# Performance work log

Hardware: AMD Instinct MI355X
Metric: run time of the kernel (lower is better)

The kernel has to match this reference:

```python
import jax, jax.numpy as jnp
import numpy as np

BLOCK_SIZE = 32
# NVFP4 decode table: index bit3 = sign, bits0-2 = magnitude code
DECODE = jnp.array([0.0, 0.5, 1.0, 1.5, 2.0, 3.0, 4.0, 6.0,
                    -0.0, -0.5, -1.0, -1.5, -2.0, -3.0, -4.0, -6.0], dtype=jnp.float32)

N_OUT, K_IN = 16384, 4096


def setup_inputs() -> dict:
    key = jax.random.key(0)
    k1, k2, k3, k4 = jax.random.split(key, 4)
    x = jax.random.normal(k1, (4, 512, K_IN), dtype=jnp.float32)
    # packed uint8 stored as int32 in [0, 256)
    weight_packed = jax.random.randint(k2, (N_OUT, K_IN // 2), 0, 256, dtype=jnp.int32)
    # per-block positive scales (block_max / 6.0 in the original)
    weight_scales = jax.random.uniform(k3, (N_OUT, K_IN // BLOCK_SIZE), dtype=jnp.float32,
                                       minval=1e-3, maxval=5e-2)
    bias = jax.random.normal(k4, (N_OUT,), dtype=jnp.float32) * 0.02
    return {"x": x, "weight_packed": weight_packed, "weight_scales": weight_scales, "bias": bias}


def _dequant(weight_packed, weight_scales):
    # unpack: low nibble -> even K index, high nibble -> odd K index
    low = DECODE[weight_packed & 15]           # [N, K//2]
    high = DECODE[(weight_packed >> 4) & 15]   # [N, K//2]
    n = weight_packed.shape[0]
    w = jnp.stack([low, high], axis=-1).reshape(n, -1)  # [N, K], interleaved
    # expand per-block scales along K
    scales = jnp.repeat(weight_scales, BLOCK_SIZE, axis=1)  # [N, K]
    return w * scales


def reference(x, weight_packed, weight_scales, bias):
    w = _dequant(weight_packed, weight_scales)            # [N, K]
    out = jnp.einsum('bsk,nk->bsn', x, w) + bias          # [B, S, N]
    # activation='gelu' -> F.gelu(approximate='tanh')
    return jax.nn.gelu(out, approximate=True)
```

## Files before the change

kernel.cpp:

```cpp
#include <hip/hip_runtime.h>
#include <hip/hip_bf16.h>

typedef short bf16x8 __attribute__((ext_vector_type(8)));
typedef float f32x4 __attribute__((ext_vector_type(4)));

#define K_DIM 4096
#define N_DIM 16384
#define M_DIM 2048
#define STRIPE 16384
#define TSTRIDE (64 * STRIPE)
#define WSB_BYTES ((size_t)N_DIM * K_DIM * 2)
#define WSA_BYTES ((size_t)M_DIM * K_DIM * 2)

__device__ __forceinline__ unsigned f2bf(float f) {
    unsigned u = __builtin_bit_cast(unsigned, f);
    u += 0x7FFFu + ((u >> 16) & 1u);
    return u >> 16;
}

__device__ __forceinline__ float dec4(unsigned c, float s) {
    unsigned mag = c & 7u;
    unsigned u = (mag >= 2u) ? ((((mag >> 1) + 126u) << 23) | ((mag & 1u) << 22))
                             : (mag == 1u ? 0x3F000000u : 0u);
    u |= (c & 8u) << 28;
    return __builtin_bit_cast(float, u) * s;
}

__device__ __forceinline__ float gelu_tanh(float v) {
    float c = v + 0.044715f * v * v * v;
    float t = tanhf(0.7978845608028654f * c);
    return 0.5f * v * (1.0f + t);
}

__global__ __launch_bounds__(256) void dequant_w(const int* __restrict__ wp,
                                                 const float* __restrict__ wsc,
                                                 unsigned char* __restrict__ dst) {
    int t = blockIdx.x * 256 + threadIdx.x;
    int n = t >> 9;
    int ck = t & 511;
    int kstep = ck >> 3, s = ck & 7;
    int nt = n >> 7, r = n & 127;

    const int4 p4 = *reinterpret_cast<const int4*>(wp + (size_t)n * (K_DIM / 2) + kstep * 32 + s * 4);
    float scale = wsc[(size_t)n * (K_DIM / 32) + kstep * 2 + (s >> 2)];

    const int pv[4] = {p4.x, p4.y, p4.z, p4.w};
    unsigned o[8];
    #pragma unroll
    for (int j = 0; j < 4; ++j) {
        unsigned b = (unsigned)pv[j] & 255u;
        o[2 * j]     = f2bf(dec4(b & 15u, scale));
        o[2 * j + 1] = f2bf(dec4((b >> 4) & 15u, scale));
    }
    uint4 v;
    v.x = o[0] | (o[1] << 16);
    v.y = o[2] | (o[3] << 16);
    v.z = o[4] | (o[5] << 16);
    v.w = o[6] | (o[7] << 16);

    size_t off = (size_t)(nt * 64 + kstep) * STRIPE
               + (size_t)r * 128 + (size_t)((s ^ (r & 7)) << 4);
    *reinterpret_cast<uint4*>(dst + off) = v;
}

__global__ __launch_bounds__(256) void conv_x(const float* __restrict__ x,
                                              unsigned char* __restrict__ dst) {
    int t = blockIdx.x * 256 + threadIdx.x;
    int m = t >> 9;
    int ck = t & 511;
    int kstep = ck >> 3, s = ck & 7;
    int mt = m >> 7, r = m & 127;

    const float4* xp = reinterpret_cast<const float4*>(x + (size_t)m * K_DIM + kstep * 64 + s * 8);
    float4 a = xp[0], b = xp[1];
    uint4 v;
    v.x = f2bf(a.x) | (f2bf(a.y) << 16);
    v.y = f2bf(a.z) | (f2bf(a.w) << 16);
    v.z = f2bf(b.x) | (f2bf(b.y) << 16);
    v.w = f2bf(b.z) | (f2bf(b.w) << 16);

    size_t off = (size_t)(mt * 64 + kstep) * STRIPE
               + (size_t)r * 128 + (size_t)((s ^ (r & 7)) << 4);
    *reinterpret_cast<uint4*>(dst + off) = v;
}


__global__ __launch_bounds__(512, 2) void gemm_bf16_256(
    const unsigned char* __restrict__ wsA,
    const unsigned char* __restrict__ wsB,
    const float* __restrict__ bias,
    float* __restrict__ out)
{
    __shared__ unsigned char lds[131072];

    int id = blockIdx.x;
    int wg = (id & 7) * 64 + (id >> 3);
    int MT = wg & 7;
    int NT = wg >> 3;

    const int tid  = threadIdx.x;
    const int lane = tid & 63;
    const int w    = tid >> 6;
    const int wm   = w >> 2;
    const int wn   = w & 3;
    const int fr   = lane & 15;
    const int fg   = lane >> 4;

    const unsigned char* gA = wsA + (size_t)(2 * MT) * TSTRIDE;
    const unsigned char* gB = wsB + (size_t)(2 * NT) * TSTRIDE;

    int addrA[8];
    #pragma unroll
    for (int mi = 0; mi < 8; ++mi) {
        int row = wm * 128 + mi * 16 + fr;
        int L = row >> 1;
        addrA[mi] = L * 128 + (((((row & 1) << 2) | fg) ^ (L & 7)) << 4);
    }
    int addrB[4];
    #pragma unroll
    for (int ni = 0; ni < 4; ++ni) {
        int row = wn * 64 + ni * 16 + fr;
        int L = row >> 1;
        addrB[ni] = L * 128 + (((((row & 1) << 2) | fg) ^ (L & 7)) << 4);
    }

    int offST[2][2];
    #pragma unroll
    for (int j = 0; j < 2; ++j) {
        int c = w * 2 + j;
        int L = c * 8 + (lane >> 3);
        int p = lane & 7;
        int sl = p ^ (L & 7);
        int h = sl >> 2, fgs = sl & 3;
        int row = 2 * L + h;
        #pragma unroll
        for (int kb = 0; kb < 2; ++kb)
            offST[j][kb] = (row >> 7) * TSTRIDE + (row & 127) * 128
                         + ((((kb << 2) | fgs) ^ (row & 7)) << 4);
    }

#define GLDS(SRC, DOFF) __builtin_amdgcn_global_load_lds(                          \
        (const __attribute__((address_space(1))) unsigned int*)(SRC),              \
        (__attribute__((address_space(3))) unsigned int*)(&lds[DOFF]), 16, 0, 0)

#define STAGE_A(KSOFF, KB, SLOT) do {                                              \
        GLDS(gA + (KSOFF) + offST[0][KB], ((SLOT) << 14) + (w * 2 + 0) * 1024);    \
        GLDS(gA + (KSOFF) + offST[1][KB], ((SLOT) << 14) + (w * 2 + 1) * 1024);    \
    } while (0)
#define STAGE_B(KSOFF, KB, SLOT) do {                                              \
        GLDS(gB + (KSOFF) + offST[0][KB], 65536 + ((SLOT) << 14) + (w * 2 + 0) * 1024); \
        GLDS(gB + (KSOFF) + offST[1][KB], 65536 + ((SLOT) << 14) + (w * 2 + 1) * 1024); \
    } while (0)

    f32x4 acc[8][4];
    #pragma unroll
    for (int mi = 0; mi < 8; ++mi)
        #pragma unroll
        for (int ni = 0; ni < 4; ++ni)
            acc[mi][ni] = (f32x4){0.f, 0.f, 0.f, 0.f};

    STAGE_A(0, 0, 0);        STAGE_B(0, 0, 0);
    STAGE_A(0, 1, 1);        STAGE_B(0, 1, 1);
    STAGE_A(STRIPE, 0, 2);   STAGE_B(STRIPE, 0, 2);
    asm volatile("s_waitcnt vmcnt(8)" ::: "memory");
    __builtin_amdgcn_sched_barrier(0);
    __builtin_amdgcn_s_barrier();
    __builtin_amdgcn_sched_barrier(0);

#define TILE_BODY(RSLOT, DO_STG, STKS, STKB, SSLOT, VMN) do {                      \
        const unsigned char* la = lds + ((RSLOT) << 14);                           \
        const unsigned char* lb = lds + 65536 + ((RSLOT) << 14);                   \
        bf16x8 bfr[4], af[4];                                                      \
        if (DO_STG) STAGE_A(STKS, STKB, SSLOT);                                    \
        _Pragma("unroll") for (int ni = 0; ni < 4; ++ni)                           \
            bfr[ni] = *reinterpret_cast<const bf16x8*>(lb + addrB[ni]);            \
        _Pragma("unroll") for (int mi = 0; mi < 4; ++mi)                           \
            af[mi] = *reinterpret_cast<const bf16x8*>(la + addrA[mi]);             \
        __builtin_amdgcn_s_setprio(1);                                             \
        _Pragma("unroll") for (int mi = 0; mi < 4; ++mi)                           \
            _Pragma("unroll") for (int ni = 0; ni < 4; ++ni)                       \
                acc[mi][ni] = __builtin_amdgcn_mfma_f32_16x16x32_bf16(             \
                    af[mi], bfr[ni], acc[mi][ni], 0, 0, 0);                        \
        __builtin_amdgcn_s_setprio(0);                                             \
        if (DO_STG) STAGE_B(STKS, STKB, SSLOT);                                    \
        _Pragma("unroll") for (int mi = 0; mi < 4; ++mi)                           \
            af[mi] = *reinterpret_cast<const bf16x8*>(la + addrA[4 + mi]);         \
        __builtin_amdgcn_s_setprio(1);                                             \
        _Pragma("unroll") for (int mi = 0; mi < 4; ++mi)                           \
            _Pragma("unroll") for (int ni = 0; ni < 4; ++ni)                       \
                acc[4 + mi][ni] = __builtin_amdgcn_mfma_f32_16x16x32_bf16(         \
                    af[mi], bfr[ni], acc[4 + mi][ni], 0, 0, 0);                    \
        __builtin_amdgcn_s_setprio(0);                                             \
        if ((VMN) >= 0) {                                                          \
            if ((VMN) == 8)      asm volatile("s_waitcnt vmcnt(8)" ::: "memory");  \
            else if ((VMN) == 4) asm volatile("s_waitcnt vmcnt(4)" ::: "memory");  \
            else                 asm volatile("s_waitcnt vmcnt(0)" ::: "memory");  \
            __builtin_amdgcn_sched_barrier(0);                                     \
            __builtin_amdgcn_s_barrier();                                          \
            __builtin_amdgcn_sched_barrier(0);                                     \
        }                                                                          \
    } while (0)

    for (int tp = 0; tp < 62; ++tp) {
        const int scur = (tp & 1) << 1;
        const int ks1 = (tp + 1) * STRIPE;
        const int ks2 = (tp + 2) * STRIPE;
        TILE_BODY(scur,     1, ks1, 1, scur ^ 3, 8);
        TILE_BODY(scur ^ 1, 1, ks2, 0, scur,     8);
    }
    TILE_BODY(0, 1, 63 * STRIPE, 1, 3, 8);
    TILE_BODY(1, 0, 0, 0, 0, 4);
    TILE_BODY(2, 0, 0, 0, 0, 0);
    TILE_BODY(3, 0, 0, 0, 0, -1);

    const int bm0 = MT * 256, bn0 = NT * 256;
    #pragma unroll
    for (int mi = 0; mi < 8; ++mi) {
        int row = bm0 + wm * 128 + mi * 16 + fg * 4;
        #pragma unroll
        for (int ni = 0; ni < 4; ++ni) {
            int col = bn0 + wn * 64 + ni * 16 + fr;
            float bv = bias[col];
            float* op = out + (size_t)row * N_DIM + col;
            #pragma unroll
            for (int q = 0; q < 4; ++q) {
                float v = acc[mi][ni][q] + bv;
                op[(size_t)q * N_DIM] = gelu_tanh(v);
            }
        }
    }
#undef TILE_BODY
#undef STAGE_A
#undef STAGE_B
#undef GLDS
}

__global__ __launch_bounds__(256, 2) void nvfp4_gemm(
    const float* __restrict__ x,
    const int*   __restrict__ wp,
    const float* __restrict__ wscale,
    const float* __restrict__ bias,
    float* __restrict__ out)
{
    __shared__ uint4  lsA[128 * 8];
    __shared__ uint4  lsB[128 * 8];
    __shared__ float2 lut[256];

    const int tid = threadIdx.x;
    {
        static const float dectab[16] = {0.f, 0.5f, 1.f, 1.5f, 2.f, 3.f, 4.f, 6.f,
                                         -0.f,-0.5f,-1.f,-1.5f,-2.f,-3.f,-4.f,-6.f};
        lut[tid] = make_float2(dectab[tid & 15], dectab[(tid >> 4) & 15]);
    }

    const int bn0 = blockIdx.x * 128;
    const int bm0 = blockIdx.y * 128;
    const int r = tid >> 1;
    const int h = tid & 1;

    const float4* xp = reinterpret_cast<const float4*>(x + (size_t)(bm0 + r) * K_DIM) + h * 8;
    const uint4*  bp = reinterpret_cast<const uint4*>(wp + (size_t)(bn0 + r) * (K_DIM / 2)) + h * 4;
    const float*  sp = wscale + (size_t)(bn0 + r) * (K_DIM / 32) + h;

    float4 ax[8];
    uint4  bx[4];
    float  scale;
    #pragma unroll
    for (int j = 0; j < 8; ++j) ax[j] = xp[j];
    #pragma unroll
    for (int q = 0; q < 4; ++q) bx[q] = bp[q];
    scale = sp[0];

    f32x4 acc[4][4];
    #pragma unroll
    for (int mi = 0; mi < 4; ++mi)
        #pragma unroll
        for (int ni = 0; ni < 4; ++ni)
            acc[mi][ni] = (f32x4){0.f, 0.f, 0.f, 0.f};

    const int lane = tid & 63;
    const int wid  = tid >> 6;
    const int wm0  = (wid >> 1) * 64;
    const int wn0  = (wid & 1) * 64;
    const int fr   = lane & 15;
    const int fg   = lane >> 4;

    __syncthreads();

    for (int kt = 0; kt < 64; ++kt) {
        #pragma unroll
        for (int j = 0; j < 4; ++j) {
            float4 f0 = ax[2 * j], f1 = ax[2 * j + 1];
            uint4 v;
            v.x = f2bf(f0.x) | (f2bf(f0.y) << 16);
            v.y = f2bf(f0.z) | (f2bf(f0.w) << 16);
            v.z = f2bf(f1.x) | (f2bf(f1.y) << 16);
            v.w = f2bf(f1.z) | (f2bf(f1.w) << 16);
            lsA[(r * 8 + h * 4 + j) ^ (r & 7)] = v;
        }
        #pragma unroll
        for (int q = 0; q < 4; ++q) {
            uint4 p = bx[q];
            float2 d0 = lut[p.x & 255];
            float2 d1 = lut[p.y & 255];
            float2 d2 = lut[p.z & 255];
            float2 d3 = lut[p.w & 255];
            uint4 v;
            v.x = f2bf(d0.x * scale) | (f2bf(d0.y * scale) << 16);
            v.y = f2bf(d1.x * scale) | (f2bf(d1.y * scale) << 16);
            v.z = f2bf(d2.x * scale) | (f2bf(d2.y * scale) << 16);
            v.w = f2bf(d3.x * scale) | (f2bf(d3.y * scale) << 16);
            lsB[(r * 8 + h * 4 + q) ^ (r & 7)] = v;
        }
        __syncthreads();

        if (kt + 1 < 64) {
            #pragma unroll
            for (int j = 0; j < 8; ++j) ax[j] = xp[(kt + 1) * 16 + j];
            #pragma unroll
            for (int q = 0; q < 4; ++q) bx[q] = bp[(kt + 1) * 8 + q];
            scale = sp[(kt + 1) * 2];
        }

        #pragma unroll
        for (int kk = 0; kk < 2; ++kk) {
            bf16x8 af[4], bfr[4];
            #pragma unroll
            for (int mi = 0; mi < 4; ++mi) {
                int row = wm0 + mi * 16 + fr;
                af[mi] = __builtin_bit_cast(bf16x8, lsA[(row * 8 + kk * 4 + fg) ^ (row & 7)]);
            }
            #pragma unroll
            for (int ni = 0; ni < 4; ++ni) {
                int row = wn0 + ni * 16 + fr;
                bfr[ni] = __builtin_bit_cast(bf16x8, lsB[(row * 8 + kk * 4 + fg) ^ (row & 7)]);
            }
            #pragma unroll
            for (int mi = 0; mi < 4; ++mi)
                #pragma unroll
                for (int ni = 0; ni < 4; ++ni)
                    acc[mi][ni] = __builtin_amdgcn_mfma_f32_16x16x32_bf16(
                        af[mi], bfr[ni], acc[mi][ni], 0, 0, 0);
        }
        __syncthreads();
    }

    #pragma unroll
    for (int mi = 0; mi < 4; ++mi) {
        int row = bm0 + wm0 + mi * 16 + fg * 4;
        #pragma unroll
        for (int ni = 0; ni < 4; ++ni) {
            int col = bn0 + wn0 + ni * 16 + fr;
            float bv = bias[col];
            float* op = out + (size_t)row * N_DIM + col;
            #pragma unroll
            for (int q = 0; q < 4; ++q) {
                float v = acc[mi][ni][q] + bv;
                op[(size_t)q * N_DIM] = gelu_tanh(v);
            }
        }
    }
}

extern "C" void kernel_launch(void* const* d_in, const int* in_sizes, int n_in,
                              void* d_out, int out_size, void* d_ws, size_t ws_size,
                              hipStream_t stream) {
    const float* x    = (const float*)d_in[0];
    const int*   wp   = (const int*)d_in[1];
    const float* wsc  = (const float*)d_in[2];
    const float* bias = (const float*)d_in[3];
    float*       out  = (float*)d_out;
    (void)in_sizes; (void)n_in; (void)out_size;

    if (ws_size >= WSB_BYTES + WSA_BYTES) {
        unsigned char* wsB = (unsigned char*)d_ws;
        unsigned char* wsA = wsB + WSB_BYTES;
        dequant_w<<<(N_DIM * (K_DIM / 8)) / 256, 256, 0, stream>>>(wp, wsc, wsB);
        conv_x<<<(M_DIM * (K_DIM / 8)) / 256, 256, 0, stream>>>(x, wsA);
        gemm_bf16_256<<<(M_DIM / 256) * (N_DIM / 256), 512, 0, stream>>>(wsA, wsB, bias, out);
    } else {
        dim3 grid(N_DIM / 128, M_DIM / 128);
        nvfp4_gemm<<<grid, 256, 0, stream>>>(x, wp, wsc, bias, out);
    }
}
```

Before: 322.3 us.

## Prefetch next tile's LDS fragments into registers during current tile's MFMAs

Software-pipelines the LDS-to-register reads in the bf16 GEMM main loop. The B fragments and the first half of the A fragments for the next k-slot are read into a second register set while the current slot's second MFMA batch runs. This hides LDS read latency behind matrix instructions. It tightens the global-load waits (vmcnt 8 to 4) so the next slot is resident one tile earlier, which may expose more global-load latency. It also raises VGPR pressure under the 2-wave occupancy bound.

```diff
diff --git a/kernel.cpp b/kernel.cpp
--- a/kernel.cpp
+++ b/kernel.cpp
@@ -152,48 +152,55 @@
         GLDS(gB + (KSOFF) + offST[1][KB], 65536 + ((SLOT) << 14) + (w * 2 + 1) * 1024); \
     } while (0)
 
+#define READ_PF(PA, PB, SLOT) do {                                                 \
+        const unsigned char* La_ = lds + ((SLOT) << 14);                           \
+        const unsigned char* Lb_ = lds + 65536 + ((SLOT) << 14);                   \
+        _Pragma("unroll") for (int ni = 0; ni < 4; ++ni)                           \
+            PB[ni] = *reinterpret_cast<const bf16x8*>(Lb_ + addrB[ni]);            \
+        _Pragma("unroll") for (int mi = 0; mi < 4; ++mi)                           \
+            PA[mi] = *reinterpret_cast<const bf16x8*>(La_ + addrA[mi]);            \
+    } while (0)
+
     f32x4 acc[8][4];
     #pragma unroll
     for (int mi = 0; mi < 8; ++mi)
         #pragma unroll
         for (int ni = 0; ni < 4; ++ni)
             acc[mi][ni] = (f32x4){0.f, 0.f, 0.f, 0.f};
+
+    bf16x8 pa0[4], pb0[4], pa1[4], pb1[4];
 
     STAGE_A(0, 0, 0);        STAGE_B(0, 0, 0);
     STAGE_A(0, 1, 1);        STAGE_B(0, 1, 1);
     STAGE_A(STRIPE, 0, 2);   STAGE_B(STRIPE, 0, 2);
-    asm volatile("s_waitcnt vmcnt(8)" ::: "memory");
+    asm volatile("s_waitcnt vmcnt(4)" ::: "memory");
     __builtin_amdgcn_sched_barrier(0);
     __builtin_amdgcn_s_barrier();
     __builtin_amdgcn_sched_barrier(0);
-
-#define TILE_BODY(RSLOT, DO_STG, STKS, STKB, SSLOT, VMN) do {                      \
+    READ_PF(pa0, pb0, 0);
+
+#define TILE_BODY(RSLOT, NSLOT, PA, PB, NPA, NPB, DO_STG, STKS, STKB, SSLOT, DO_PF, VMN) do { \
         const unsigned char* la = lds + ((RSLOT) << 14);                           \
-        const unsigned char* lb = lds + 65536 + ((RSLOT) << 14);                   \
-        bf16x8 bfr[4], af[4];                                                      \
+        bf16x8 ka[4];                                                              \
         if (DO_STG) STAGE_A(STKS, STKB, SSLOT);                                    \
-        _Pragma("unroll") for (int ni = 0; ni < 4; ++ni)                           \
-            bfr[ni] = *reinterpret_cast<const bf16x8*>(lb + addrB[ni]);            \
         _Pragma("unroll") for (int mi = 0; mi < 4; ++mi)                           \
-            af[mi] = *reinterpret_cast<const bf16x8*>(la + addrA[mi]);             \
+            ka[mi] = *reinterpret_cast<const bf16x8*>(la + addrA[4 + mi]);         \
         __builtin_amdgcn_s_setprio(1);                                             \
         _Pragma("unroll") for (int mi = 0; mi < 4; ++mi)                           \
             _Pragma("unroll") for (int ni = 0; ni < 4; ++ni)                       \
                 acc[mi][ni] = __builtin_amdgcn_mfma_f32_16x16x32_bf16(             \
-                    af[mi], bfr[ni], acc[mi][ni], 0, 0, 0);                        \
+                    PA[mi], PB[ni], acc[mi][ni], 0, 0, 0);                         \
         __builtin_amdgcn_s_setprio(0);                                             \
         if (DO_STG) STAGE_B(STKS, STKB, SSLOT);                                    \
-        _Pragma("unroll") for (int mi = 0; mi < 4; ++mi)                           \
-            af[mi] = *reinterpret_cast<const bf16x8*>(la + addrA[4 + mi]);         \
+        if (DO_PF) READ_PF(NPA, NPB, NSLOT);                                       \
         __builtin_amdgcn_s_setprio(1);                                             \
         _Pragma("unroll") for (int mi = 0; mi < 4; ++mi)                           \
             _Pragma("unroll") for (int ni = 0; ni < 4; ++ni)                       \
                 acc[4 + mi][ni] = __builtin_amdgcn_mfma_f32_16x16x32_bf16(         \
-                    af[mi], bfr[ni], acc[4 + mi][ni], 0, 0, 0);                    \
+                    ka[mi], PB[ni], acc[4 + mi][ni], 0, 0, 0);                     \
         __builtin_amdgcn_s_setprio(0);                                             \
         if ((VMN) >= 0) {                                                          \
-            if ((VMN) == 8)      asm volatile("s_waitcnt vmcnt(8)" ::: "memory");  \
-            else if ((VMN) == 4) asm volatile("s_waitcnt vmcnt(4)" ::: "memory");  \
+            if ((VMN) == 4)      asm volatile("s_waitcnt vmcnt(4)" ::: "memory");  \
             else                 asm volatile("s_waitcnt vmcnt(0)" ::: "memory");  \
             __builtin_amdgcn_sched_barrier(0);                                     \
             __builtin_amdgcn_s_barrier();                                          \
@@ -205,13 +212,13 @@
         const int scur = (tp & 1) << 1;
         const int ks1 = (tp + 1) * STRIPE;
         const int ks2 = (tp + 2) * STRIPE;
-        TILE_BODY(scur,     1, ks1, 1, scur ^ 3, 8);
-        TILE_BODY(scur ^ 1, 1, ks2, 0, scur,     8);
-    }
-    TILE_BODY(0, 1, 63 * STRIPE, 1, 3, 8);
-    TILE_BODY(1, 0, 0, 0, 0, 4);
-    TILE_BODY(2, 0, 0, 0, 0, 0);
-    TILE_BODY(3, 0, 0, 0, 0, -1);
+        TILE_BODY(scur,     scur ^ 1, pa0, pb0, pa1, pb1, 1, ks1, 1, scur ^ 3, 1, 4);
+        TILE_BODY(scur ^ 1, scur ^ 2, pa1, pb1, pa0, pb0, 1, ks2, 0, scur,     1, 4);
+    }
+    TILE_BODY(0, 1, pa0, pb0, pa1, pb1, 1, 63 * STRIPE, 1, 3, 1, 4);
+    TILE_BODY(1, 2, pa1, pb1, pa0, pb0, 0, 0, 0, 0, 1, 0);
+    TILE_BODY(2, 3, pa0, pb0, pa1, pb1, 0, 0, 0, 0, 1, 0);
+    TILE_BODY(3, 0, pa1, pb1, pa0, pb0, 0, 0, 0, 0, 0, -1);
 
     const int bm0 = MT * 256, bn0 = NT * 256;
     #pragma unroll
@@ -230,6 +237,7 @@
         }
     }
 #undef TILE_BODY
+#undef READ_PF
 #undef STAGE_A
 #undef STAGE_B
 #undef GLDS
```

Measured after the change: 319.8 us. No clear change (-0.8%).

## Restructure GEMM LDS pipeline to double-buffered 64-K tiles with register prefetch

Applied to the files above, without the earlier changes.

The bf16 GEMM main loop changes from a four-slot LDS ring of 32-K half-tiles with staggered vmcnt waits to two 64 KB slots, each holding a full 64-K tile for A and B. Each tile is split in two halves. The first half's fragments are prefetched into registers before the barrier, so MFMAs on them overlap the wait for the next tile's global-to-LDS loads. This cuts the number of barriers per K step and the per-tile issue overhead. In exchange it uses more VGPRs for the prefetched fragments, which could hurt occupancy at two blocks per CU, and it waits with vmcnt(0) on the full next tile.

```diff
diff --git a/kernel.cpp b/kernel.cpp
--- a/kernel.cpp
+++ b/kernel.cpp
@@ -112,44 +112,54 @@
     int addrA[8];
     #pragma unroll
     for (int mi = 0; mi < 8; ++mi) {
-        int row = wm * 128 + mi * 16 + fr;
-        int L = row >> 1;
-        addrA[mi] = L * 128 + (((((row & 1) << 2) | fg) ^ (L & 7)) << 4);
+        int r = mi * 16 + fr;
+        int L = r >> 1;
+        addrA[mi] = wm * 16384 + L * 128 + (((((r & 1) << 2) | fg) ^ (L & 7)) << 4);
     }
     int addrB[4];
     #pragma unroll
     for (int ni = 0; ni < 4; ++ni) {
         int row = wn * 64 + ni * 16 + fr;
-        int L = row >> 1;
-        addrB[ni] = L * 128 + (((((row & 1) << 2) | fg) ^ (L & 7)) << 4);
-    }
-
-    int offST[2][2];
+        int H = row >> 7, r = row & 127;
+        int L = r >> 1;
+        addrB[ni] = 32768 + H * 16384 + L * 128
+                  + (((((r & 1) << 2) | fg) ^ (L & 7)) << 4);
+    }
+
+    int srcoff[2], dstoff[2];
     #pragma unroll
     for (int j = 0; j < 2; ++j) {
-        int c = w * 2 + j;
-        int L = c * 8 + (lane >> 3);
-        int p = lane & 7;
-        int sl = p ^ (L & 7);
-        int h = sl >> 2, fgs = sl & 3;
-        int row = 2 * L + h;
-        #pragma unroll
-        for (int kb = 0; kb < 2; ++kb)
-            offST[j][kb] = (row >> 7) * TSTRIDE + (row & 127) * 128
-                         + ((((kb << 2) | fgs) ^ (row & 7)) << 4);
+        int S = (w * 2 + j) * 64 + lane;
+        int kkS = S >> 9;
+        int L = (S >> 3) & 63;
+        int p = S & 7;
+        int hp = p ^ (L & 7);
+        int row = 2 * L + (hp >> 2);
+        int kq = hp & 3;
+        srcoff[j] = row * 128 + ((((kkS << 2) | kq) ^ (row & 7)) << 4);
+        dstoff[j] = (w * 2 + j) * 1024 + lane * 16;
     }
 
 #define GLDS(SRC, DOFF) __builtin_amdgcn_global_load_lds(                          \
         (const __attribute__((address_space(1))) unsigned int*)(SRC),              \
         (__attribute__((address_space(3))) unsigned int*)(&lds[DOFF]), 16, 0, 0)
 
-#define STAGE_A(KSOFF, KB, SLOT) do {                                              \
-        GLDS(gA + (KSOFF) + offST[0][KB], ((SLOT) << 14) + (w * 2 + 0) * 1024);    \
-        GLDS(gA + (KSOFF) + offST[1][KB], ((SLOT) << 14) + (w * 2 + 1) * 1024);    \
+#define STAGE_TILE(KT, SS) do {                                                    \
+        size_t ko_ = (size_t)(KT) * STRIPE;                                        \
+        _Pragma("unroll") for (int j = 0; j < 2; ++j) {                            \
+            GLDS(gA + ko_ + srcoff[j],            ((SS) << 16) +         dstoff[j]); \
+            GLDS(gA + TSTRIDE + ko_ + srcoff[j],  ((SS) << 16) + 16384 + dstoff[j]); \
+            GLDS(gB + ko_ + srcoff[j],            ((SS) << 16) + 32768 + dstoff[j]); \
+            GLDS(gB + TSTRIDE + ko_ + srcoff[j],  ((SS) << 16) + 49152 + dstoff[j]); \
+        }                                                                          \
     } while (0)
-#define STAGE_B(KSOFF, KB, SLOT) do {                                              \
-        GLDS(gB + (KSOFF) + offST[0][KB], 65536 + ((SLOT) << 14) + (w * 2 + 0) * 1024); \
-        GLDS(gB + (KSOFF) + offST[1][KB], 65536 + ((SLOT) << 14) + (w * 2 + 1) * 1024); \
+
+#define READ_PF(SS) do {                                                           \
+        const unsigned char* Lp_ = lds + ((SS) << 16);                             \
+        _Pragma("unroll") for (int ni = 0; ni < 4; ++ni)                           \
+            pb[ni] = *reinterpret_cast<const bf16x8*>(Lp_ + addrB[ni]);            \
+        _Pragma("unroll") for (int mi = 0; mi < 8; ++mi)                           \
+            pa[mi] = *reinterpret_cast<const bf16x8*>(Lp_ + addrA[mi]);            \
     } while (0)
 
     f32x4 acc[8][4];
@@ -159,59 +169,55 @@
         for (int ni = 0; ni < 4; ++ni)
             acc[mi][ni] = (f32x4){0.f, 0.f, 0.f, 0.f};
 
-    STAGE_A(0, 0, 0);        STAGE_B(0, 0, 0);
-    STAGE_A(0, 1, 1);        STAGE_B(0, 1, 1);
-    STAGE_A(STRIPE, 0, 2);   STAGE_B(STRIPE, 0, 2);
-    asm volatile("s_waitcnt vmcnt(8)" ::: "memory");
+    bf16x8 pa[8], pb[4];
+
+    STAGE_TILE(0, 0);
+    asm volatile("s_waitcnt vmcnt(0)" ::: "memory");
     __builtin_amdgcn_sched_barrier(0);
     __builtin_amdgcn_s_barrier();
     __builtin_amdgcn_sched_barrier(0);
-
-#define TILE_BODY(RSLOT, DO_STG, STKS, STKB, SSLOT, VMN) do {                      \
-        const unsigned char* la = lds + ((RSLOT) << 14);                           \
-        const unsigned char* lb = lds + 65536 + ((RSLOT) << 14);                   \
-        bf16x8 bfr[4], af[4];                                                      \
-        if (DO_STG) STAGE_A(STKS, STKB, SSLOT);                                    \
+    READ_PF(0);
+
+#define TILE_BODY(SS, DO_NXT, KT1) do {                                            \
+        const unsigned char* ls_ = lds + ((SS) << 16);                             \
+        bf16x8 a1[8], b1[4];                                                       \
+        if (DO_NXT) STAGE_TILE(KT1, (SS) ^ 1);                                     \
         _Pragma("unroll") for (int ni = 0; ni < 4; ++ni)                           \
-            bfr[ni] = *reinterpret_cast<const bf16x8*>(lb + addrB[ni]);            \
-        _Pragma("unroll") for (int mi = 0; mi < 4; ++mi)                           \
-            af[mi] = *reinterpret_cast<const bf16x8*>(la + addrA[mi]);             \
+            b1[ni] = *reinterpret_cast<const bf16x8*>(ls_ + addrB[ni] + 8192);     \
+        _Pragma("unroll") for (int mi = 0; mi < 8; ++mi)                           \
+            a1[mi] = *reinterpret_cast<const bf16x8*>(ls_ + addrA[mi] + 8192);     \
         __builtin_amdgcn_s_setprio(1);                                             \
-        _Pragma("unroll") for (int mi = 0; mi < 4; ++mi)                           \
+        _Pragma("unroll") for (int mi = 0; mi < 8; ++mi)                           \
             _Pragma("unroll") for (int ni = 0; ni < 4; ++ni)                       \
                 acc[mi][ni] = __builtin_amdgcn_mfma_f32_16x16x32_bf16(             \
-                    af[mi], bfr[ni], acc[mi][ni], 0, 0, 0);                        \
+                    pa[mi], pb[ni], acc[mi][ni], 0, 0, 0);                         \
         __builtin_amdgcn_s_setprio(0);                                             \
-        if (DO_STG) STAGE_B(STKS, STKB, SSLOT);                                    \
-        _Pragma("unroll") for (int mi = 0; mi < 4; ++mi)                           \
-            af[mi] = *reinterpret_cast<const bf16x8*>(la + addrA[4 + mi]);         \
+        if (DO_NXT) {                                                              \
+            asm volatile("s_waitcnt vmcnt(0)" ::: "memory");                       \
+            __builtin_amdgcn_sched_barrier(0);                                     \
+            __builtin_amdgcn_s_barrier();                                          \
+            __builtin_amdgcn_sched_barrier(0);                                     \
+            READ_PF((SS) ^ 1);                                                     \
+        }                                                                          \
         __builtin_amdgcn_s_setprio(1);                                             \
-        _Pragma("unroll") for (int mi = 0; mi < 4; ++mi)                           \
+        _Pragma("unroll") for (int mi = 0; mi < 8; ++mi)                           \
             _Pragma("unroll") for (int ni = 0; ni < 4; ++ni)                       \
-                acc[4 + mi][ni] = __builtin_amdgcn_mfma_f32_16x16x32_bf16(         \
-                    af[mi], bfr[ni], acc[4 + mi][ni], 0, 0, 0);                    \
+                acc[mi][ni] = __builtin_amdgcn_mfma_f32_16x16x32_bf16(             \
+                    a1[mi], b1[ni], acc[mi][ni], 0, 0, 0);                         \
         __builtin_amdgcn_s_setprio(0);                                             \
-        if ((VMN) >= 0) {                                                          \
-            if ((VMN) == 8)      asm volatile("s_waitcnt vmcnt(8)" ::: "memory");  \
-            else if ((VMN) == 4) asm volatile("s_waitcnt vmcnt(4)" ::: "memory");  \
-            else                 asm volatile("s_waitcnt vmcnt(0)" ::: "memory");  \
+        if (DO_NXT) {                                                              \
             __builtin_amdgcn_sched_barrier(0);                                     \
             __builtin_amdgcn_s_barrier();                                          \
             __builtin_amdgcn_sched_barrier(0);                                     \
         }                                                                          \
     } while (0)
 
-    for (int tp = 0; tp < 62; ++tp) {
-        const int scur = (tp & 1) << 1;
-        const int ks1 = (tp + 1) * STRIPE;
-        const int ks2 = (tp + 2) * STRIPE;
-        TILE_BODY(scur,     1, ks1, 1, scur ^ 3, 8);
-        TILE_BODY(scur ^ 1, 1, ks2, 0, scur,     8);
-    }
-    TILE_BODY(0, 1, 63 * STRIPE, 1, 3, 8);
-    TILE_BODY(1, 0, 0, 0, 0, 4);
-    TILE_BODY(2, 0, 0, 0, 0, 0);
-    TILE_BODY(3, 0, 0, 0, 0, -1);
+    for (int tp = 0; tp < 31; ++tp) {
+        TILE_BODY(0, 1, 2 * tp + 1);
+        TILE_BODY(1, 1, 2 * tp + 2);
+    }
+    TILE_BODY(0, 1, 63);
+    TILE_BODY(1, 0, 0);
 
     const int bm0 = MT * 256, bn0 = NT * 256;
     #pragma unroll
@@ -230,8 +236,8 @@
         }
     }
 #undef TILE_BODY
-#undef STAGE_A
-#undef STAGE_B
+#undef READ_PF
+#undef STAGE_TILE
 #undef GLDS
 }
 
```

Measured after the change: 522.8 us. 62.2% more time.

## Double GEMM workgroup to 1024 threads with smaller per-wave tiles; fast GELU

Applied to the files above, without the earlier changes.

The GEMM workgroup grows from 8 to 16 waves. Each wave now covers a 64x64 output sub-tile instead of 128x64, halving accumulator registers per wave, and each thread stages one 16-byte global-to-LDS load per operand per k-step instead of two. The wait counts and the staging order are changed to match, and the setprio hints are removed. Separately, the epilogue tanh is replaced with an exp2-plus-reciprocal formula using hardware approximations. The aim is more waves to hide latency and a cheaper epilogue, at the cost of more LDS reads per MFMA and more barrier participants.

```diff
diff --git a/kernel.cpp b/kernel.cpp
--- a/kernel.cpp
+++ b/kernel.cpp
@@ -26,10 +26,15 @@
     return __builtin_bit_cast(float, u) * s;
 }
 
+__device__ __forceinline__ float fexp2(float x) {
+    float r; asm("v_exp_f32 %0, %1" : "=v"(r) : "v"(x)); return r;
+}
 __device__ __forceinline__ float gelu_tanh(float v) {
     float c = v + 0.044715f * v * v * v;
-    float t = tanhf(0.7978845608028654f * c);
-    return 0.5f * v * (1.0f + t);
+    float x = fminf(-2.3022084f * c, 80.0f);
+    float t = fexp2(x);
+    float th = (1.0f - t) * __builtin_amdgcn_rcpf(1.0f + t);
+    return 0.5f * v * (1.0f + th);
 }
 
 __global__ __launch_bounds__(256) void dequant_w(const int* __restrict__ wp,
@@ -85,7 +90,7 @@
 }
 
 
-__global__ __launch_bounds__(512, 2) void gemm_bf16_256(
+__global__ __launch_bounds__(1024, 4) void gemm_bf16_256(
     const unsigned char* __restrict__ wsA,
     const unsigned char* __restrict__ wsB,
     const float* __restrict__ bias,
@@ -109,10 +114,10 @@
     const unsigned char* gA = wsA + (size_t)(2 * MT) * TSTRIDE;
     const unsigned char* gB = wsB + (size_t)(2 * NT) * TSTRIDE;
 
-    int addrA[8];
-    #pragma unroll
-    for (int mi = 0; mi < 8; ++mi) {
-        int row = wm * 128 + mi * 16 + fr;
+    int addrA[4];
+    #pragma unroll
+    for (int mi = 0; mi < 4; ++mi) {
+        int row = wm * 64 + mi * 16 + fr;
         int L = row >> 1;
         addrA[mi] = L * 128 + (((((row & 1) << 2) | fg) ^ (L & 7)) << 4);
     }
@@ -124,37 +129,31 @@
         addrB[ni] = L * 128 + (((((row & 1) << 2) | fg) ^ (L & 7)) << 4);
     }
 
-    int offST[2][2];
-    #pragma unroll
-    for (int j = 0; j < 2; ++j) {
-        int c = w * 2 + j;
-        int L = c * 8 + (lane >> 3);
-        int p = lane & 7;
-        int sl = p ^ (L & 7);
-        int h = sl >> 2, fgs = sl & 3;
-        int row = 2 * L + h;
+    int offST[2];
+    {
+        int S = tid;
+        int L = S >> 3;
+        int p = S & 7;
+        int hp = p ^ (L & 7);
+        int row = 2 * L + (hp >> 2);
+        int kq = hp & 3;
         #pragma unroll
         for (int kb = 0; kb < 2; ++kb)
-            offST[j][kb] = (row >> 7) * TSTRIDE + (row & 127) * 128
-                         + ((((kb << 2) | fgs) ^ (row & 7)) << 4);
-    }
+            offST[kb] = (row >> 7) * TSTRIDE + (row & 127) * 128
+                      + ((((kb << 2) | kq) ^ (row & 7)) << 4);
+    }
+    const int dstST = tid * 16;
 
 #define GLDS(SRC, DOFF) __builtin_amdgcn_global_load_lds(                          \
         (const __attribute__((address_space(1))) unsigned int*)(SRC),              \
         (__attribute__((address_space(3))) unsigned int*)(&lds[DOFF]), 16, 0, 0)
 
-#define STAGE_A(KSOFF, KB, SLOT) do {                                              \
-        GLDS(gA + (KSOFF) + offST[0][KB], ((SLOT) << 14) + (w * 2 + 0) * 1024);    \
-        GLDS(gA + (KSOFF) + offST[1][KB], ((SLOT) << 14) + (w * 2 + 1) * 1024);    \
-    } while (0)
-#define STAGE_B(KSOFF, KB, SLOT) do {                                              \
-        GLDS(gB + (KSOFF) + offST[0][KB], 65536 + ((SLOT) << 14) + (w * 2 + 0) * 1024); \
-        GLDS(gB + (KSOFF) + offST[1][KB], 65536 + ((SLOT) << 14) + (w * 2 + 1) * 1024); \
-    } while (0)
-
-    f32x4 acc[8][4];
-    #pragma unroll
-    for (int mi = 0; mi < 8; ++mi)
+#define STAGE_A(KSOFF, KB, SLOT) GLDS(gA + (KSOFF) + offST[KB], ((SLOT) << 15) + dstST)
+#define STAGE_B(KSOFF, KB, SLOT) GLDS(gB + (KSOFF) + offST[KB], ((SLOT) << 15) + 16384 + dstST)
+
+    f32x4 acc[4][4];
+    #pragma unroll
+    for (int mi = 0; mi < 4; ++mi)
         #pragma unroll
         for (int ni = 0; ni < 4; ++ni)
             acc[mi][ni] = (f32x4){0.f, 0.f, 0.f, 0.f};
@@ -162,38 +161,27 @@
     STAGE_A(0, 0, 0);        STAGE_B(0, 0, 0);
     STAGE_A(0, 1, 1);        STAGE_B(0, 1, 1);
     STAGE_A(STRIPE, 0, 2);   STAGE_B(STRIPE, 0, 2);
-    asm volatile("s_waitcnt vmcnt(8)" ::: "memory");
+    asm volatile("s_waitcnt vmcnt(2)" ::: "memory");
     __builtin_amdgcn_sched_barrier(0);
     __builtin_amdgcn_s_barrier();
     __builtin_amdgcn_sched_barrier(0);
 
 #define TILE_BODY(RSLOT, DO_STG, STKS, STKB, SSLOT, VMN) do {                      \
-        const unsigned char* la = lds + ((RSLOT) << 14);                           \
-        const unsigned char* lb = lds + 65536 + ((RSLOT) << 14);                   \
-        bf16x8 bfr[4], af[4];                                                      \
+        const unsigned char* la = lds + ((RSLOT) << 15);                           \
+        const unsigned char* lb = la + 16384;                                      \
+        bf16x8 af[4], bf[4];                                                       \
         if (DO_STG) STAGE_A(STKS, STKB, SSLOT);                                    \
         _Pragma("unroll") for (int ni = 0; ni < 4; ++ni)                           \
-            bfr[ni] = *reinterpret_cast<const bf16x8*>(lb + addrB[ni]);            \
+            bf[ni] = *reinterpret_cast<const bf16x8*>(lb + addrB[ni]);             \
         _Pragma("unroll") for (int mi = 0; mi < 4; ++mi)                           \
             af[mi] = *reinterpret_cast<const bf16x8*>(la + addrA[mi]);             \
-        __builtin_amdgcn_s_setprio(1);                                             \
+        if (DO_STG) STAGE_B(STKS, STKB, SSLOT);                                    \
         _Pragma("unroll") for (int mi = 0; mi < 4; ++mi)                           \
             _Pragma("unroll") for (int ni = 0; ni < 4; ++ni)                       \
                 acc[mi][ni] = __builtin_amdgcn_mfma_f32_16x16x32_bf16(             \
-                    af[mi], bfr[ni], acc[mi][ni], 0, 0, 0);                        \
-        __builtin_amdgcn_s_setprio(0);                                             \
-        if (DO_STG) STAGE_B(STKS, STKB, SSLOT);                                    \
-        _Pragma("unroll") for (int mi = 0; mi < 4; ++mi)                           \
-            af[mi] = *reinterpret_cast<const bf16x8*>(la + addrA[4 + mi]);         \
-        __builtin_amdgcn_s_setprio(1);                                             \
-        _Pragma("unroll") for (int mi = 0; mi < 4; ++mi)                           \
-            _Pragma("unroll") for (int ni = 0; ni < 4; ++ni)                       \
-                acc[4 + mi][ni] = __builtin_amdgcn_mfma_f32_16x16x32_bf16(         \
-                    af[mi], bfr[ni], acc[4 + mi][ni], 0, 0, 0);                    \
-        __builtin_amdgcn_s_setprio(0);                                             \
+                    af[mi], bf[ni], acc[mi][ni], 0, 0, 0);                         \
         if ((VMN) >= 0) {                                                          \
-            if ((VMN) == 8)      asm volatile("s_waitcnt vmcnt(8)" ::: "memory");  \
-            else if ((VMN) == 4) asm volatile("s_waitcnt vmcnt(4)" ::: "memory");  \
+            if ((VMN) == 2)      asm volatile("s_waitcnt vmcnt(2)" ::: "memory");  \
             else                 asm volatile("s_waitcnt vmcnt(0)" ::: "memory");  \
             __builtin_amdgcn_sched_barrier(0);                                     \
             __builtin_amdgcn_s_barrier();                                          \
@@ -205,18 +193,18 @@
         const int scur = (tp & 1) << 1;
         const int ks1 = (tp + 1) * STRIPE;
         const int ks2 = (tp + 2) * STRIPE;
-        TILE_BODY(scur,     1, ks1, 1, scur ^ 3, 8);
-        TILE_BODY(scur ^ 1, 1, ks2, 0, scur,     8);
-    }
-    TILE_BODY(0, 1, 63 * STRIPE, 1, 3, 8);
-    TILE_BODY(1, 0, 0, 0, 0, 4);
+        TILE_BODY(scur,     1, ks1, 1, scur ^ 3, 2);
+        TILE_BODY(scur ^ 1, 1, ks2, 0, scur,     2);
+    }
+    TILE_BODY(0, 1, 63 * STRIPE, 1, 3, 2);
+    TILE_BODY(1, 0, 0, 0, 0, 2);
     TILE_BODY(2, 0, 0, 0, 0, 0);
     TILE_BODY(3, 0, 0, 0, 0, -1);
 
     const int bm0 = MT * 256, bn0 = NT * 256;
     #pragma unroll
-    for (int mi = 0; mi < 8; ++mi) {
-        int row = bm0 + wm * 128 + mi * 16 + fg * 4;
+    for (int mi = 0; mi < 4; ++mi) {
+        int row = bm0 + wm * 64 + mi * 16 + fg * 4;
         #pragma unroll
         for (int ni = 0; ni < 4; ++ni) {
             int col = bn0 + wn * 64 + ni * 16 + fr;
@@ -377,7 +365,7 @@
         unsigned char* wsA = wsB + WSB_BYTES;
         dequant_w<<<(N_DIM * (K_DIM / 8)) / 256, 256, 0, stream>>>(wp, wsc, wsB);
         conv_x<<<(M_DIM * (K_DIM / 8)) / 256, 256, 0, stream>>>(x, wsA);
-        gemm_bf16_256<<<(M_DIM / 256) * (N_DIM / 256), 512, 0, stream>>>(wsA, wsB, bias, out);
+        gemm_bf16_256<<<(M_DIM / 256) * (N_DIM / 256), 1024, 0, stream>>>(wsA, wsB, bias, out);
     } else {
         dim3 grid(N_DIM / 128, M_DIM / 128);
         nvfp4_gemm<<<grid, 256, 0, stream>>>(x, wp, wsc, bias, out);
```

After: 324.0 us. No clear change (+0.5%).
